# Performance work log

Measured on AMD Instinct MI355X. Metric: run time of the kernel, lower is better.

The kernel has to match this reference:

```python
import jax, jax.numpy as jnp
import numpy as np

N_HEAD = 16
HEAD_DIM = 64
WINDOW = 256
ROPE_BASE = 10000.0


def _rope_cos_sin(seq_len, dtype):
    inv_freq = 1.0 / (ROPE_BASE ** (jnp.arange(0, HEAD_DIM, 2, dtype=jnp.float32) / HEAD_DIM))
    t = jnp.arange(seq_len, dtype=jnp.float32)
    freqs = jnp.outer(t, inv_freq)                      # [S, D/2]
    emb = jnp.concatenate([freqs, freqs], axis=-1)      # [S, D]
    return jnp.cos(emb).astype(dtype), jnp.sin(emb).astype(dtype)


def _rotate_half(x):
    x1, x2 = jnp.split(x, 2, axis=-1)
    return jnp.concatenate([-x2, x1], axis=-1)


def _apply_rope(x, cos, sin):
    # x: [B, H, S, D]; cos/sin: [S, D]
    return x * cos[None, None, :, :] + _rotate_half(x) * sin[None, None, :, :]


def setup_inputs() -> dict:
    key = jax.random.key(0)
    ks = jax.random.split(key, 5)
    B, S, E = 2, 2048, 1024
    scale = 1.0 / np.sqrt(E)
    return {
        "x": jax.random.normal(ks[0], (B, S, E), dtype=jnp.float32),
        "Wq": jax.random.normal(ks[1], (E, E), dtype=jnp.float32) * scale,
        "Wk": jax.random.normal(ks[2], (E, E), dtype=jnp.float32) * scale,
        "Wv": jax.random.normal(ks[3], (E, E), dtype=jnp.float32) * scale,
        "Wo": jax.random.normal(ks[4], (E, E), dtype=jnp.float32) * scale,
    }


def reference(x, Wq, Wk, Wv, Wo):
    B, S, E = x.shape
    # QKV projections (nn.Linear: x @ W.T), split heads -> [B, H, S, D]
    def proj(W):
        return (x @ W.T).reshape(B, S, N_HEAD, HEAD_DIM).transpose(0, 2, 1, 3)
    q, k, v = proj(Wq), proj(Wk), proj(Wv)

    cos, sin = _rope_cos_sin(S, x.dtype)
    q = _apply_rope(q, cos, sin)
    k = _apply_rope(k, cos, sin)

    # banded causal mask: attend iff 0 <= i - j < WINDOW
    pos = jnp.arange(S)
    rel = pos[:, None] - pos[None, :]
    allowed = (rel >= 0) & (rel < WINDOW)                # [S, S]

    scale = 1.0 / np.sqrt(HEAD_DIM)
    att = jnp.einsum("bhqd,bhkd->bhqk", q, k) * scale    # [B, H, S, S]
    att = jnp.where(allowed[None, None, :, :], att, -jnp.inf)
    att = jax.nn.softmax(att.astype(jnp.float32), axis=-1).astype(x.dtype)
    y = jnp.einsum("bhqk,bhkd->bhqd", att, v)
    y = y.transpose(0, 2, 1, 3).reshape(B, S, E)
    return y @ Wo.T
```

## Files before the change

kernel.cpp:

```cpp
#include <hip/hip_runtime.h>
#include <cstdint>
#include <cstddef>

#define AS1 __attribute__((address_space(1)))
#define AS3 __attribute__((address_space(3)))

typedef __attribute__((ext_vector_type(4))) float f32x4;
typedef __attribute__((ext_vector_type(2))) float f32x2;
typedef __attribute__((ext_vector_type(8))) short bf16x8;
typedef unsigned short u16;
typedef unsigned int u32;

#define B_ 2
#define S_ 2048
#define E_ 1024
#define H_ 16
#define D_ 64
#define M_ 4096

__device__ __forceinline__ u16 f2bf(float f) {
  union { float f; u32 u; } v; v.f = f;
  u32 u = v.u;
  u32 r = (u + 0x7FFFu + ((u >> 16) & 1u)) >> 16;
  return (u16)r;
}
__device__ __forceinline__ float bf2f(u16 h) {
  union { u32 u; float f; } v; v.u = ((u32)h) << 16;
  return v.f;
}

__device__ __forceinline__ void gl2lds16(const void* g, void* l) {
  __builtin_amdgcn_global_load_lds((const AS1 void*)g, (AS3 void*)l, 16, 0, 0);
}

__global__ __launch_bounds__(256) void prep_kernel(
    const float* __restrict__ x, const float* __restrict__ wq,
    const float* __restrict__ wk, const float* __restrict__ wv,
    const float* __restrict__ wo,
    u16* __restrict__ xb, u16* __restrict__ wqkv, u16* __restrict__ wob,
    float* __restrict__ cstab)
{
  int idx = blockIdx.x * 256 + threadIdx.x;
  const int NX4 = (M_ * E_) / 4;
  const int NW4 = (E_ * E_) / 4;
  const int CONV_TOTAL = NX4 + 4 * NW4;
  if (idx < CONV_TOTAL) {
    const float* src; u16* dst; int off;
    if (idx < NX4)                { src = x;  dst = xb;              off = idx; }
    else if (idx < NX4 + NW4)     { src = wq; dst = wqkv;            off = idx - NX4; }
    else if (idx < NX4 + 2 * NW4) { src = wk; dst = wqkv + E_ * E_;  off = idx - NX4 - NW4; }
    else if (idx < NX4 + 3 * NW4) { src = wv; dst = wqkv + 2 * E_ * E_; off = idx - NX4 - 2 * NW4; }
    else                          { src = wo; dst = wob;             off = idx - NX4 - 3 * NW4; }
    float4 v = reinterpret_cast<const float4*>(src)[off];
    ushort4 o;
    o.x = f2bf(v.x); o.y = f2bf(v.y); o.z = f2bf(v.z); o.w = f2bf(v.w);
    reinterpret_cast<ushort4*>(dst)[off] = o;
  } else if (idx < CONV_TOTAL + S_ * 32) {
    int e = idx - CONV_TOTAL;
    int s = e >> 5, i = e & 31;
    double invf = pow(10000.0, -(double)i / 32.0);
    double ang = (double)s * invf;
    cstab[e * 2]     = (float)cos(ang);
    cstab[e * 2 + 1] = (float)sin(ang);
  }
}

#define BARR  asm volatile("s_barrier" ::: "memory")
#define LGKM0 asm volatile("s_waitcnt lgkmcnt(0)" ::: "memory")
#define VMC6  asm volatile("s_waitcnt vmcnt(6)" ::: "memory")
#define VMC0  asm volatile("s_waitcnt vmcnt(0)" ::: "memory")

__global__ __launch_bounds__(512, 2) void gemm_qkv(
    const u16* __restrict__ A, const u16* __restrict__ Bm,
    u16* __restrict__ q_out, u16* __restrict__ k_out, u16* __restrict__ vt_out,
    const float* __restrict__ cstab)
{
  __shared__ __align__(16) u16 lds8[65536];
  const int tid = threadIdx.x;
  const int w = tid >> 6, l = tid & 63;
  const int lr = l & 15, lg = l >> 4;
  const int wm = w >> 2, wn = w & 3;

  int bid = blockIdx.x;
  int wg = (bid & 7) * 24 + (bid >> 3);
  int mt = wg / 12, nt = wg % 12;

  const int rA = w * 32 + (l >> 2);
  const int koff = ((l & 3) ^ ((l >> 3) & 3)) * 8;
  const u16* aSrc = A + (size_t)(mt * 256 + rA) * 1024 + koff;
  const u16* bSrc = Bm + (size_t)(nt * 256 + rA) * 1024 + koff;
  const int aswz = 16 * (lg ^ ((lr >> 1) & 3));

#define STG(isB, ks, bb, t) do { \
    const u16* s_ = ((isB) ? bSrc : aSrc) + (t) * 64 + (ks) * 32; \
    u16* d_ = &lds8[(((bb)*2 + (isB))*2 + (ks)) * 8192 + w * 1024]; \
    gl2lds16(s_, d_); \
    gl2lds16(s_ + 16 * 1024, d_ + 512); \
  } while (0)

#define LDA8(qm, ks, bb) do { \
    const char* sl_ = (const char*)lds8 + (((bb)*2)*2 + (ks)) * 16384; \
    _Pragma("unroll") for (int mf_ = 0; mf_ < 4; ++mf_) { \
      int row_ = wm * 128 + (qm) * 64 + mf_ * 16 + lr; \
      av[mf_] = *(const bf16x8*)(sl_ + row_ * 64 + aswz); \
    } } while (0)

#define LDB8(ks, bb) do { \
    const char* sl_ = (const char*)lds8 + (((bb)*2 + 1)*2 + (ks)) * 16384; \
    _Pragma("unroll") for (int nf_ = 0; nf_ < 4; ++nf_) { \
      int row_ = wn * 64 + nf_ * 16 + lr; \
      bv[nf_] = *(const bf16x8*)(sl_ + row_ * 64 + aswz); \
    } } while (0)

#define MMA16(qm) do { \
    __builtin_amdgcn_s_setprio(1); \
    _Pragma("unroll") for (int mf_ = 0; mf_ < 4; ++mf_) \
    _Pragma("unroll") for (int nf_ = 0; nf_ < 4; ++nf_) \
      acc[(qm)*4 + mf_][nf_] = __builtin_amdgcn_mfma_f32_16x16x32_bf16( \
          av[mf_], bv[nf_], acc[(qm)*4 + mf_][nf_], 0, 0, 0); \
    __builtin_amdgcn_s_setprio(0); \
  } while (0)

  f32x4 acc[8][4];
#pragma unroll
  for (int i = 0; i < 8; ++i)
#pragma unroll
    for (int j = 0; j < 4; ++j) acc[i][j] = (f32x4){0.f, 0.f, 0.f, 0.f};
  bf16x8 av[4], bv[4];

  STG(0, 0, 0, 0); STG(1, 0, 0, 0); STG(0, 1, 0, 0); STG(1, 1, 0, 0);
  STG(1, 0, 1, 1); STG(0, 0, 1, 1); STG(1, 1, 1, 1);
  VMC6; BARR;

  for (int i = 0; i < 8; ++i) {
    LDA8(0, 0, 0); LDB8(0, 0);
    STG(0, 1, 1, 2 * i + 1);
    BARR; LGKM0; MMA16(0); BARR;
    LDA8(1, 0, 0);
    if (i < 7) STG(1, 0, 0, 2 * i + 2);
    BARR; LGKM0; MMA16(1); BARR;
    LDA8(0, 1, 0); LDB8(1, 0);
    if (i < 7) STG(0, 0, 0, 2 * i + 2);
    BARR; LGKM0; MMA16(0); BARR;
    LDA8(1, 1, 0);
    if (i < 7) STG(1, 1, 0, 2 * i + 2);
    BARR; LGKM0; MMA16(1);
    if (i < 7) { VMC6; } else { VMC0; }
    BARR;
    LDA8(0, 0, 1); LDB8(0, 1);
    if (i < 7) STG(0, 1, 0, 2 * i + 2);
    BARR; LGKM0; MMA16(0); BARR;
    LDA8(1, 0, 1);
    if (i < 7) STG(1, 0, 1, 2 * i + 3);
    BARR; LGKM0; MMA16(1); BARR;
    LDA8(0, 1, 1); LDB8(1, 1);
    if (i < 7) STG(0, 0, 1, 2 * i + 3);
    BARR; LGKM0; MMA16(0); BARR;
    LDA8(1, 1, 1);
    if (i < 7) STG(1, 1, 1, 2 * i + 3);
    BARR; LGKM0; MMA16(1);
    if (i < 7) VMC6;
    BARR;
  }
  __syncthreads();

  int n0 = nt * 256 + wn * 64;
  int wsel = n0 >> 10;
  int hh = (n0 >> 6) & 15;
  int stile = mt * 256 + wm * 128;
  int b = stile >> 11;
  int s0 = stile & 2047;

  if (wsel == 2) {
#pragma unroll
    for (int mf = 0; mf < 8; ++mf) {
      int s = s0 + mf * 16 + lg * 4;
#pragma unroll
      for (int nf = 0; nf < 4; ++nf) {
        int d = nf * 16 + lr;
        ushort4 pk;
        pk.x = f2bf(acc[mf][nf][0]); pk.y = f2bf(acc[mf][nf][1]);
        pk.z = f2bf(acc[mf][nf][2]); pk.w = f2bf(acc[mf][nf][3]);
        *reinterpret_cast<ushort4*>(
            vt_out + ((size_t)(b * 16 + hh) * 64 + d) * 2048 + s) = pk;
      }
    }
  } else {
    u16* gout = (wsel == 0 ? q_out : k_out) +
                ((size_t)(b * 16 + hh) * 2048 + s0) * 64;
    u16* lt = &lds8[w * 4352];
    const f32x2* cst = (const f32x2*)cstab;
#pragma unroll
    for (int P = 0; P < 2; ++P) {
#pragma unroll
      for (int mf_ = 0; mf_ < 4; ++mf_) {
        int mf = P * 4 + mf_;
        int rl = mf_ * 16 + lg * 4;
#pragma unroll
        for (int rr = 0; rr < 4; ++rr) {
          int s = s0 + P * 64 + rl + rr;
#pragma unroll
          for (int nf_ = 0; nf_ < 2; ++nf_) {
            int ii = nf_ * 16 + lr;
            f32x2 cs = cst[s * 32 + ii];
            float a = acc[mf][nf_][rr], b2 = acc[mf][nf_ + 2][rr];
            lt[(rl + rr) * 68 + ii]      = f2bf(a * cs.x - b2 * cs.y);
            lt[(rl + rr) * 68 + 32 + ii] = f2bf(b2 * cs.x + a * cs.y);
          }
        }
      }
      LGKM0;
      {
        int trl = l >> 3, tcc = l & 7;
#pragma unroll
        for (int it = 0; it < 8; ++it) {
          int row = it * 8 + trl;
          bf16x8 v = *(const bf16x8*)(lt + row * 68 + tcc * 8);
          *(bf16x8*)(gout + (size_t)(P * 64 + row) * 64 + tcc * 8) = v;
        }
      }
      LGKM0;
    }
  }
#undef STG
#undef LDA8
#undef LDB8
#undef MMA16
}

__global__ __launch_bounds__(256) void gemm_out(
    const u16* __restrict__ A, const u16* __restrict__ Bm,
    float* __restrict__ f_out)
{
  __shared__ __align__(16) u16 smem[16384];
  u16* lA = smem;
  u16* lB = smem + 8192;
  const int tid = threadIdx.x;
  const int w = tid >> 6, l = tid & 63;
  const int lr = l & 15, lg = l >> 4;
  const int mt = blockIdx.y, nt = blockIdx.x;
  const int woffm = (w >> 1) * 64, woffn = (w & 1) * 64;

  const int srow = l >> 3;
  const int scol = ((l & 7) ^ srow) * 8;
  const u16* Abase = A + (size_t)(mt * 128) * 1024;
  const u16* Bbase = Bm + (size_t)(nt * 128) * 1024;

  f32x4 acc[4][4];
#pragma unroll
  for (int i = 0; i < 4; ++i)
#pragma unroll
    for (int j = 0; j < 4; ++j) acc[i][j] = (f32x4){0.f, 0.f, 0.f, 0.f};

  for (int kt = 0; kt < 1024; kt += 64) {
    __syncthreads();
#pragma unroll
    for (int i = 0; i < 4; ++i) {
      int ch = w * 4 + i;
      int row = ch * 8 + srow;
      gl2lds16(Abase + row * 1024 + kt + scol, &lA[ch * 512]);
      gl2lds16(Bbase + row * 1024 + kt + scol, &lB[ch * 512]);
    }
    __syncthreads();
#pragma unroll
    for (int kk = 0; kk < 2; ++kk) {
      bf16x8 av[4], bv[4];
#pragma unroll
      for (int mf = 0; mf < 4; ++mf) {
        int row = woffm + mf * 16 + lr;
        int byteoff = row * 128 + ((kk * 64 + lg * 16) ^ ((row & 7) << 4));
        av[mf] = *(const bf16x8*)((const char*)lA + byteoff);
      }
#pragma unroll
      for (int nf = 0; nf < 4; ++nf) {
        int row = woffn + nf * 16 + lr;
        int byteoff = row * 128 + ((kk * 64 + lg * 16) ^ ((row & 7) << 4));
        bv[nf] = *(const bf16x8*)((const char*)lB + byteoff);
      }
#pragma unroll
      for (int mf = 0; mf < 4; ++mf)
#pragma unroll
        for (int nf = 0; nf < 4; ++nf)
          acc[mf][nf] = __builtin_amdgcn_mfma_f32_16x16x32_bf16(
              av[mf], bv[nf], acc[mf][nf], 0, 0, 0);
    }
  }

#pragma unroll
  for (int mf = 0; mf < 4; ++mf) {
    int m = mt * 128 + woffm + mf * 16 + lg * 4;
#pragma unroll
    for (int nf = 0; nf < 4; ++nf) {
      int n = nt * 128 + woffn + nf * 16 + lr;
#pragma unroll
      for (int rr = 0; rr < 4; ++rr)
        f_out[(size_t)(m + rr) * 1024 + n] = acc[mf][nf][rr];
    }
  }
}

__global__ __launch_bounds__(256) void attn_kernel(
    const u16* __restrict__ qb, const u16* __restrict__ kb,
    const u16* __restrict__ vt, u16* __restrict__ yb)
{
  int blk = blockIdx.x;
  int qt = blk & 31, h = (blk >> 5) & 15, b = blk >> 9;
  int w = threadIdx.x >> 6, l = threadIdx.x & 63;
  int lr = l & 15, lg = l >> 4;
  int qbase = qt * 64 + w * 16;

  const u16* Q  = qb + ((size_t)(b * 16 + h) * 2048) * 64;
  const u16* Kp = kb + ((size_t)(b * 16 + h) * 2048) * 64;
  const u16* Vp = vt + ((size_t)(b * 16 + h) * 64) * 2048;

  __shared__ __align__(16) u16 lds_p[4][16 * 40];
  u16* myp = &lds_p[w][0];

  bf16x8 aq0 = *(const bf16x8*)(Q + (size_t)(qbase + lr) * 64 + lg * 8);
  bf16x8 aq1 = *(const bf16x8*)(Q + (size_t)(qbase + lr) * 64 + 32 + lg * 8);

  f32x4 o[4];
#pragma unroll
  for (int i = 0; i < 4; ++i) o[i] = (f32x4){0.f, 0.f, 0.f, 0.f};
  float mrun[4], lsum[4];
#pragma unroll
  for (int r = 0; r < 4; ++r) { mrun[r] = -1e30f; lsum[r] = 0.f; }

  int kstart = qbase - 255; if (kstart < 0) kstart = 0;
  kstart &= ~31;
  int kend = qbase + 16;
  const float scale = 0.125f;

  for (int kt = kstart; kt < kend; kt += 32) {
    bf16x8 bk0a = *(const bf16x8*)(Kp + (size_t)(kt + lr) * 64 + lg * 8);
    bf16x8 bk0b = *(const bf16x8*)(Kp + (size_t)(kt + lr) * 64 + 32 + lg * 8);
    bf16x8 bk1a = *(const bf16x8*)(Kp + (size_t)(kt + 16 + lr) * 64 + lg * 8);
    bf16x8 bk1b = *(const bf16x8*)(Kp + (size_t)(kt + 16 + lr) * 64 + 32 + lg * 8);
    f32x4 s0 = (f32x4){0.f, 0.f, 0.f, 0.f};
    f32x4 s1 = (f32x4){0.f, 0.f, 0.f, 0.f};
    s0 = __builtin_amdgcn_mfma_f32_16x16x32_bf16(aq0, bk0a, s0, 0, 0, 0);
    s0 = __builtin_amdgcn_mfma_f32_16x16x32_bf16(aq1, bk0b, s0, 0, 0, 0);
    s1 = __builtin_amdgcn_mfma_f32_16x16x32_bf16(aq0, bk1a, s1, 0, 0, 0);
    s1 = __builtin_amdgcn_mfma_f32_16x16x32_bf16(aq1, bk1b, s1, 0, 0, 0);

    float p0[4], p1[4];
#pragma unroll
    for (int r = 0; r < 4; ++r) {
      int q = qbase + lg * 4 + r;
      int k0 = kt + lr, k1 = k0 + 16;
      int r0 = q - k0, r1 = q - k1;
      float v0 = (r0 >= 0 && r0 < 256) ? s0[r] * scale : -1e30f;
      float v1 = (r1 >= 0 && r1 < 256) ? s1[r] * scale : -1e30f;
      float pmax = fmaxf(v0, v1);
      if (!__all(pmax <= mrun[r] + 8.0f)) {
        float mx = pmax;
        mx = fmaxf(mx, __shfl_xor(mx, 1));
        mx = fmaxf(mx, __shfl_xor(mx, 2));
        mx = fmaxf(mx, __shfl_xor(mx, 4));
        mx = fmaxf(mx, __shfl_xor(mx, 8));
        float mnew = fmaxf(mrun[r], mx);
        float f = __expf(mrun[r] - mnew);
        mrun[r] = mnew;
        lsum[r] *= f;
#pragma unroll
        for (int nf = 0; nf < 4; ++nf) o[nf][r] *= f;
      }
      p0[r] = __expf(v0 - mrun[r]);
      p1[r] = __expf(v1 - mrun[r]);
      lsum[r] += p0[r] + p1[r];
    }

#pragma unroll
    for (int r = 0; r < 4; ++r) {
      myp[(lg * 4 + r) * 40 + lr]      = f2bf(p0[r]);
      myp[(lg * 4 + r) * 40 + 16 + lr] = f2bf(p1[r]);
    }
    asm volatile("s_waitcnt lgkmcnt(0)" ::: "memory");
    bf16x8 pa = *(const bf16x8*)((const char*)myp + lr * 80 + lg * 16);
    asm volatile("s_waitcnt lgkmcnt(0)" ::: "memory");

#pragma unroll
    for (int df = 0; df < 4; ++df) {
      bf16x8 vv = *(const bf16x8*)(Vp + (size_t)(df * 16 + lr) * 2048 + kt + lg * 8);
      o[df] = __builtin_amdgcn_mfma_f32_16x16x32_bf16(pa, vv, o[df], 0, 0, 0);
    }
  }

  float lrun[4];
#pragma unroll
  for (int r = 0; r < 4; ++r) {
    float sm = lsum[r];
    sm += __shfl_xor(sm, 1);
    sm += __shfl_xor(sm, 2);
    sm += __shfl_xor(sm, 4);
    sm += __shfl_xor(sm, 8);
    lrun[r] = 1.f / sm;
  }
#pragma unroll
  for (int df = 0; df < 4; ++df)
#pragma unroll
    for (int r = 0; r < 4; ++r) {
      int s = qbase + lg * 4 + r;
      int d = df * 16 + lr;
      yb[((size_t)(b * 2048 + s)) * 1024 + h * 64 + d] = f2bf(o[df][r] * lrun[r]);
    }
}

extern "C" void kernel_launch(void* const* d_in, const int* in_sizes, int n_in,
                              void* d_out, int out_size, void* d_ws, size_t ws_size,
                              hipStream_t stream) {
  const float* x  = (const float*)d_in[0];
  const float* wq = (const float*)d_in[1];
  const float* wk = (const float*)d_in[2];
  const float* wv = (const float*)d_in[3];
  const float* wo = (const float*)d_in[4];

  char* ws = (char*)d_ws;
  const size_t MB = 1u << 20;
  if (ws_size < 49 * MB) return;
  u16*   xb   = (u16*)(ws);
  u16*   wqkv = (u16*)(ws + 8 * MB);
  u16*   wob  = (u16*)(ws + 14 * MB);
  u16*   qb   = (u16*)(ws + 16 * MB);
  u16*   kb   = (u16*)(ws + 24 * MB);
  u16*   vt   = (u16*)(ws + 32 * MB);
  u16*   yb   = (u16*)(ws + 40 * MB);
  float* cst  = (float*)(ws + 48 * MB);
  float* out  = (float*)d_out;

  prep_kernel<<<8448, 256, 0, stream>>>(x, wq, wk, wv, wo, xb, wqkv, wob, cst);
  gemm_qkv<<<192, 512, 0, stream>>>(xb, wqkv, qb, kb, vt, cst);
  attn_kernel<<<1024, 256, 0, stream>>>(qb, kb, vt, yb);
  gemm_out<<<dim3(8, 32), 256, 0, stream>>>(yb, wob, out);
}
```

Before: 179.2 us.

## Compute transposed scores so P stays in registers, skipping LDS round-trip

The attention kernel now computes S^T (K as the A operand, Q as B) with a permuted K row mapping, so each lane holds eight consecutive key probabilities for one query. These are packed directly into the bf16x8 operand of the PV MFMA, removing the LDS write/read and the waitcnt barriers. Softmax state becomes one scalar per lane, reduced with two cross-group shuffles instead of four per row. Output is written as packed 4-element vector stores. The risk is correctness of the key permutation relative to the V-tile layout.

```diff
diff --git a/kernel.cpp b/kernel.cpp
--- a/kernel.cpp
+++ b/kernel.cpp
@@ -308,102 +308,92 @@
   int w = threadIdx.x >> 6, l = threadIdx.x & 63;
   int lr = l & 15, lg = l >> 4;
   int qbase = qt * 64 + w * 16;
+  int sq = qbase + lr;
 
   const u16* Q  = qb + ((size_t)(b * 16 + h) * 2048) * 64;
   const u16* Kp = kb + ((size_t)(b * 16 + h) * 2048) * 64;
   const u16* Vp = vt + ((size_t)(b * 16 + h) * 64) * 2048;
 
-  __shared__ __align__(16) u16 lds_p[4][16 * 40];
-  u16* myp = &lds_p[w][0];
-
-  bf16x8 aq0 = *(const bf16x8*)(Q + (size_t)(qbase + lr) * 64 + lg * 8);
-  bf16x8 aq1 = *(const bf16x8*)(Q + (size_t)(qbase + lr) * 64 + 32 + lg * 8);
+  bf16x8 aq0 = *(const bf16x8*)(Q + (size_t)sq * 64 + lg * 8);
+  bf16x8 aq1 = *(const bf16x8*)(Q + (size_t)sq * 64 + 32 + lg * 8);
 
   f32x4 o[4];
 #pragma unroll
   for (int i = 0; i < 4; ++i) o[i] = (f32x4){0.f, 0.f, 0.f, 0.f};
-  float mrun[4], lsum[4];
-#pragma unroll
-  for (int r = 0; r < 4; ++r) { mrun[r] = -1e30f; lsum[r] = 0.f; }
+  float mrun = -1e30f, lsum = 0.f;
 
   int kstart = qbase - 255; if (kstart < 0) kstart = 0;
   kstart &= ~31;
   int kend = qbase + 16;
   const float scale = 0.125f;
+  const int fperm = ((lr >> 2) * 8) + (lr & 3);
 
   for (int kt = kstart; kt < kend; kt += 32) {
-    bf16x8 bk0a = *(const bf16x8*)(Kp + (size_t)(kt + lr) * 64 + lg * 8);
-    bf16x8 bk0b = *(const bf16x8*)(Kp + (size_t)(kt + lr) * 64 + 32 + lg * 8);
-    bf16x8 bk1a = *(const bf16x8*)(Kp + (size_t)(kt + 16 + lr) * 64 + lg * 8);
-    bf16x8 bk1b = *(const bf16x8*)(Kp + (size_t)(kt + 16 + lr) * 64 + 32 + lg * 8);
+    const u16* k0p = Kp + (size_t)(kt + fperm) * 64;
+    const u16* k1p = Kp + (size_t)(kt + fperm + 4) * 64;
+    bf16x8 ka0 = *(const bf16x8*)(k0p + lg * 8);
+    bf16x8 ka1 = *(const bf16x8*)(k0p + 32 + lg * 8);
+    bf16x8 kb0 = *(const bf16x8*)(k1p + lg * 8);
+    bf16x8 kb1 = *(const bf16x8*)(k1p + 32 + lg * 8);
     f32x4 s0 = (f32x4){0.f, 0.f, 0.f, 0.f};
     f32x4 s1 = (f32x4){0.f, 0.f, 0.f, 0.f};
-    s0 = __builtin_amdgcn_mfma_f32_16x16x32_bf16(aq0, bk0a, s0, 0, 0, 0);
-    s0 = __builtin_amdgcn_mfma_f32_16x16x32_bf16(aq1, bk0b, s0, 0, 0, 0);
-    s1 = __builtin_amdgcn_mfma_f32_16x16x32_bf16(aq0, bk1a, s1, 0, 0, 0);
-    s1 = __builtin_amdgcn_mfma_f32_16x16x32_bf16(aq1, bk1b, s1, 0, 0, 0);
-
-    float p0[4], p1[4];
-#pragma unroll
-    for (int r = 0; r < 4; ++r) {
-      int q = qbase + lg * 4 + r;
-      int k0 = kt + lr, k1 = k0 + 16;
-      int r0 = q - k0, r1 = q - k1;
-      float v0 = (r0 >= 0 && r0 < 256) ? s0[r] * scale : -1e30f;
-      float v1 = (r1 >= 0 && r1 < 256) ? s1[r] * scale : -1e30f;
-      float pmax = fmaxf(v0, v1);
-      if (!__all(pmax <= mrun[r] + 8.0f)) {
-        float mx = pmax;
-        mx = fmaxf(mx, __shfl_xor(mx, 1));
-        mx = fmaxf(mx, __shfl_xor(mx, 2));
-        mx = fmaxf(mx, __shfl_xor(mx, 4));
-        mx = fmaxf(mx, __shfl_xor(mx, 8));
-        float mnew = fmaxf(mrun[r], mx);
-        float f = __expf(mrun[r] - mnew);
-        mrun[r] = mnew;
-        lsum[r] *= f;
-#pragma unroll
-        for (int nf = 0; nf < 4; ++nf) o[nf][r] *= f;
-      }
-      p0[r] = __expf(v0 - mrun[r]);
-      p1[r] = __expf(v1 - mrun[r]);
-      lsum[r] += p0[r] + p1[r];
-    }
-
-#pragma unroll
-    for (int r = 0; r < 4; ++r) {
-      myp[(lg * 4 + r) * 40 + lr]      = f2bf(p0[r]);
-      myp[(lg * 4 + r) * 40 + 16 + lr] = f2bf(p1[r]);
-    }
-    asm volatile("s_waitcnt lgkmcnt(0)" ::: "memory");
-    bf16x8 pa = *(const bf16x8*)((const char*)myp + lr * 80 + lg * 16);
-    asm volatile("s_waitcnt lgkmcnt(0)" ::: "memory");
+    s0 = __builtin_amdgcn_mfma_f32_16x16x32_bf16(ka0, aq0, s0, 0, 0, 0);
+    s0 = __builtin_amdgcn_mfma_f32_16x16x32_bf16(ka1, aq1, s0, 0, 0, 0);
+    s1 = __builtin_amdgcn_mfma_f32_16x16x32_bf16(kb0, aq0, s1, 0, 0, 0);
+    s1 = __builtin_amdgcn_mfma_f32_16x16x32_bf16(kb1, aq1, s1, 0, 0, 0);
+
+    float p[8];
+    float pmax = -1e30f;
+#pragma unroll
+    for (int j = 0; j < 8; ++j) {
+      float sv = (j < 4) ? s0[j] : s1[j - 4];
+      int rel = sq - (kt + lg * 8 + j);
+      p[j] = (rel >= 0 && rel < 256) ? sv * scale : -1e30f;
+      pmax = fmaxf(pmax, p[j]);
+    }
+    if (!__all(pmax <= mrun + 8.0f)) {
+      float mx = fmaxf(pmax, __shfl_xor(pmax, 16));
+      mx = fmaxf(mx, __shfl_xor(mx, 32));
+      float mnew = fmaxf(mrun, mx);
+      float f = __expf(mrun - mnew);
+      mrun = mnew;
+      lsum *= f;
+#pragma unroll
+      for (int df = 0; df < 4; ++df) o[df] *= f;
+    }
+    float sumt = 0.f;
+#pragma unroll
+    for (int j = 0; j < 8; ++j) {
+      p[j] = __expf(p[j] - mrun);
+      sumt += p[j];
+    }
+    lsum += sumt;
+
+    union { u32 wds[4]; bf16x8 v; } pk;
+#pragma unroll
+    for (int j2 = 0; j2 < 4; ++j2)
+      pk.wds[j2] = (u32)f2bf(p[2 * j2]) | ((u32)f2bf(p[2 * j2 + 1]) << 16);
 
 #pragma unroll
     for (int df = 0; df < 4; ++df) {
       bf16x8 vv = *(const bf16x8*)(Vp + (size_t)(df * 16 + lr) * 2048 + kt + lg * 8);
-      o[df] = __builtin_amdgcn_mfma_f32_16x16x32_bf16(pa, vv, o[df], 0, 0, 0);
-    }
-  }
-
-  float lrun[4];
-#pragma unroll
-  for (int r = 0; r < 4; ++r) {
-    float sm = lsum[r];
-    sm += __shfl_xor(sm, 1);
-    sm += __shfl_xor(sm, 2);
-    sm += __shfl_xor(sm, 4);
-    sm += __shfl_xor(sm, 8);
-    lrun[r] = 1.f / sm;
-  }
-#pragma unroll
-  for (int df = 0; df < 4; ++df)
-#pragma unroll
-    for (int r = 0; r < 4; ++r) {
-      int s = qbase + lg * 4 + r;
-      int d = df * 16 + lr;
-      yb[((size_t)(b * 2048 + s)) * 1024 + h * 64 + d] = f2bf(o[df][r] * lrun[r]);
-    }
+      o[df] = __builtin_amdgcn_mfma_f32_16x16x32_bf16(vv, pk.v, o[df], 0, 0, 0);
+    }
+  }
+
+  float sm = lsum;
+  sm += __shfl_xor(sm, 16);
+  sm += __shfl_xor(sm, 32);
+  float inv = 1.f / sm;
+
+  u16* dst = yb + ((size_t)(b * 2048 + sq)) * 1024 + h * 64 + lg * 4;
+#pragma unroll
+  for (int df = 0; df < 4; ++df) {
+    ushort4 pkq;
+    pkq.x = f2bf(o[df][0] * inv); pkq.y = f2bf(o[df][1] * inv);
+    pkq.z = f2bf(o[df][2] * inv); pkq.w = f2bf(o[df][3] * inv);
+    *reinterpret_cast<ushort4*>(dst + df * 16) = pkq;
+  }
 }
 
 extern "C" void kernel_launch(void* const* d_in, const int* in_sizes, int n_in,
```

Measured after the change: 181.0 us. No clear change (+1.0%).
